# Kernel tuning notes

Measured on AMD Instinct MI355X. Metric: run time of the kernel, lower is better.

The kernel has to match this reference:

```python
import jax, jax.numpy as jnp
import numpy as np
import math

INC, OUTC, N, STRIDE = 128, 256, 9, 1
B, H, W = 8, 64, 64
EPS = 1e-5


def setup_inputs() -> dict:
    key = jax.random.key(0)
    k0, k1, k2, k3 = jax.random.split(key, 4)
    x = jax.random.normal(k0, (B, INC, H, W), jnp.float32)
    # p_conv: 3x3 conv inc -> 2N (torch inits weight=0; use small random so offsets are nontrivial)
    pw = jax.random.normal(k1, (2 * N, INC, 3, 3), jnp.float32) * 0.01
    pb = jax.random.normal(k2, (2 * N,), jnp.float32) * 0.01
    # final 1x1 conv inc -> outc (bias=None in the module), BN affine params
    cw = jax.random.normal(k3, (OUTC, INC, 1, 1), jnp.float32) * (1.0 / math.sqrt(INC))
    gamma = jnp.ones((OUTC,), jnp.float32)
    beta = jnp.zeros((OUTC,), jnp.float32)
    return dict(x=x, pw=pw, pb=pb, cw=cw, gamma=gamma, beta=beta)


def _akconv(x, pw, pb, cw, gamma, beta):
    b, c, Hx, Wx = x.shape
    # offset = p_conv(x): 3x3 conv, padding 1, stride STRIDE -> (b, 2N, h, w)
    offset = jax.lax.conv_general_dilated(
        x, pw, window_strides=(STRIDE, STRIDE), padding=((1, 1), (1, 1)),
        dimension_numbers=("NCHW", "OIHW", "NCHW")) + pb[None, :, None, None]
    h, w = offset.shape[2], offset.shape[3]

    # p_n: N points on unit circle (x=cos, y=sin), concat -> (2N,)
    angles = jnp.linspace(0.0, 2.0 * math.pi, N + 1)[:-1]
    p_n = jnp.concatenate([jnp.cos(angles), jnp.sin(angles)])  # (2N,)

    # p_0: base grid positions, (2N, h, w)
    gx = jnp.broadcast_to((jnp.arange(h, dtype=jnp.float32) * STRIDE)[:, None], (h, w))
    gy = jnp.broadcast_to((jnp.arange(w, dtype=jnp.float32) * STRIDE)[None, :], (h, w))
    p0 = jnp.concatenate([jnp.broadcast_to(gx[None], (N, h, w)),
                          jnp.broadcast_to(gy[None], (N, h, w))], axis=0)

    p = (offset + p_n[None, :, None, None] + p0[None]).transpose(0, 2, 3, 1)  # (b,h,w,2N)
    px, py = p[..., :N], p[..., N:]

    fx = jnp.floor(jax.lax.stop_gradient(px))  # q is detached in the original
    fy = jnp.floor(jax.lax.stop_gradient(py))
    q_ltx = jnp.clip(fx, 0, Hx - 1)
    q_lty = jnp.clip(fy, 0, Wx - 1)
    q_rbx = jnp.clip(fx + 1.0, 0, Hx - 1)
    q_rby = jnp.clip(fy + 1.0, 0, Wx - 1)
    pxc = jnp.clip(px, 0, Hx - 1)
    pyc = jnp.clip(py, 0, Wx - 1)

    g_lt = (1.0 + (q_ltx - pxc)) * (1.0 + (q_lty - pyc))
    g_rb = (1.0 - (q_rbx - pxc)) * (1.0 - (q_rby - pyc))
    g_lb = (1.0 + (q_ltx - pxc)) * (1.0 - (q_rby - pyc))
    g_rt = (1.0 - (q_rbx - pxc)) * (1.0 + (q_lty - pyc))

    x_flat = x.reshape(b, c, Hx * Wx)

    def gather(qx, qy):
        idx = (qx * Wx + qy).astype(jnp.int32).reshape(b, -1)  # (b, h*w*N)
        xg = jax.vmap(lambda xf, ix: xf[:, ix])(x_flat, idx)    # (b, c, h*w*N)
        return xg.reshape(b, c, h, w, N)

    x_off = (g_lt[:, None] * gather(q_ltx, q_lty)
             + g_rb[:, None] * gather(q_rbx, q_rby)
             + g_lb[:, None] * gather(q_ltx, q_rby)
             + g_rt[:, None] * gather(q_rbx, q_lty))  # (b,c,h,w,N)

    x_off = x_off.reshape(b, c, h, w * N)  # 'b c h w n -> b c h (w n)'

    # 1x1 conv (no bias) + BatchNorm (training-mode batch stats) + SiLU
    y = jnp.einsum("bchw,oc->bohw", x_off, cw[:, :, 0, 0])
    mean = jnp.mean(y, axis=(0, 2, 3), keepdims=True)
    var = jnp.var(y, axis=(0, 2, 3), keepdims=True)
    yn = (y - mean) * jax.lax.rsqrt(var + EPS)
    yn = yn * gamma[None, :, None, None] + beta[None, :, None, None]
    return yn * jax.nn.sigmoid(yn)


def reference(x, pw, pb, cw, gamma, beta):
    return _akconv(x, pw, pb, cw, gamma, beta)
```

## Files before the change

### kernel.cpp

```cpp
#include <hip/hip_runtime.h>
#include <math.h>

#define INC   128
#define OUTC  256
#define NPTS  9
#define BATCH 8
#define HDIM  64
#define WDIM  64
#define HW    4096
#define JLB   36864
#define JTOT  294912
#define NTOTF 294912.0f

typedef __bf16 bf16x8 __attribute__((ext_vector_type(8)));
typedef float  f32x4  __attribute__((ext_vector_type(4)));

__global__ void k_cvt_cw(const float* __restrict__ cw, __bf16* __restrict__ cwb) {
    int i = blockIdx.x * 256 + threadIdx.x;
    if (i < OUTC * INC) cwb[i] = (__bf16)cw[i];
}

__global__ __launch_bounds__(256) void k_transpose(
        const float* __restrict__ x, __bf16* __restrict__ xTb) {
    __shared__ __bf16 t[64 * 128];
    char* tb = (char*)t;
    int b   = blockIdx.x >> 6;
    int hw0 = (blockIdx.x & 63) << 6;
    int tid = threadIdx.x;
    int lane = tid & 63;
    int cq  = tid >> 6;
    const float* xb = x + b * (INC * HW);
    #pragma unroll
    for (int cc = 0; cc < INC; cc += 4) {
        int c = cc + cq;
        float v = xb[c * HW + hw0 + lane];
        *(__bf16*)(tb + lane * 256 + ((2 * c) ^ ((lane & 15) << 4))) = (__bf16)v;
    }
    __syncthreads();
    __bf16* ob = xTb + ((size_t)b * HW + hw0) * INC;
    #pragma unroll
    for (int i = 0; i < 4; ++i) {
        int chunk = i * 256 + tid;
        int hw  = chunk >> 4;
        int c16 = chunk & 15;
        bf16x8 vv = *(bf16x8*)(tb + hw * 256 + ((c16 * 16) ^ ((hw & 15) << 4)));
        *(bf16x8*)(ob + hw * INC + c16 * 8) = vv;
    }
}

__global__ __launch_bounds__(256) void k_prep(
        const float* __restrict__ x, const float* __restrict__ pw,
        const float* __restrict__ pb, int4* __restrict__ sidx,
        float4* __restrict__ sw) {
    int n  = blockIdx.x >> 7;
    int sp = ((blockIdx.x & 127) << 8) + threadIdx.x;
    int b  = sp >> 12;
    int hh = (sp >> 6) & 63;
    int ww = sp & 63;

    __shared__ float pwl[INC * 9 * 2];
    for (int i = threadIdx.x; i < INC * 9; i += 256) {
        pwl[i * 2 + 0] = pw[n * (INC * 9) + i];
        pwl[i * 2 + 1] = pw[(n + 9) * (INC * 9) + i];
    }
    __syncthreads();

    const float* xb = x + b * (INC * HW);
    float ax = 0.f, ay = 0.f;
    for (int c = 0; c < INC; ++c) {
        const float* xc = xb + c * HW;
        const float* pc = pwl + c * 18;
        #pragma unroll
        for (int ky = 0; ky < 3; ++ky) {
            int yy = hh - 1 + ky;
            #pragma unroll
            for (int kx = 0; kx < 3; ++kx) {
                int xx = ww - 1 + kx;
                float v = ((unsigned)yy < 64u && (unsigned)xx < 64u)
                            ? xc[yy * 64 + xx] : 0.f;
                int k = ky * 3 + kx;
                ax = fmaf(v, pc[k * 2 + 0], ax);
                ay = fmaf(v, pc[k * 2 + 1], ay);
            }
        }
    }
    ax += pb[n];
    ay += pb[n + 9];

    const float TWO_PI = 6.28318530717958647692f;
    float ang = (float)n * (TWO_PI / 9.0f);
    float px = ax + cosf(ang) + (float)hh;
    float py = ay + sinf(ang) + (float)ww;
    float fx = floorf(px), fy = floorf(py);
    float ltx = fminf(fmaxf(fx,        0.f), 63.f);
    float lty = fminf(fmaxf(fy,        0.f), 63.f);
    float rbx = fminf(fmaxf(fx + 1.f,  0.f), 63.f);
    float rby = fminf(fmaxf(fy + 1.f,  0.f), 63.f);
    float pxc = fminf(fmaxf(px,        0.f), 63.f);
    float pyc = fminf(fmaxf(py,        0.f), 63.f);
    float glt = (1.f + ltx - pxc) * (1.f + lty - pyc);
    float grb = (1.f - rbx + pxc) * (1.f - rby + pyc);
    float glb = (1.f + ltx - pxc) * (1.f - rby + pyc);
    float grt = (1.f - rbx + pxc) * (1.f + lty - pyc);

    int j = b * JLB + (hh * 64 + ww) * 9 + n;
    sidx[j] = make_int4((int)ltx * 64 + (int)lty,
                        (int)rbx * 64 + (int)rby,
                        (int)ltx * 64 + (int)rby,
                        (int)rbx * 64 + (int)lty);
    sw[j] = make_float4(glt, grb, glb, grt);
}

template <bool WRITE>
__global__ __launch_bounds__(256, 2) void k_gemm(
        const __bf16* __restrict__ xTb, const __bf16* __restrict__ cwb,
        const int4* __restrict__ sidx, const float4* __restrict__ sw,
        const float* __restrict__ scaleb, const float* __restrict__ shiftb,
        float* __restrict__ gstat, float* __restrict__ out) {
    __shared__ uint4 xoffT4[64 * 256 / 16];
    __shared__ float saux[512];
    char* xoffT = (char*)xoffT4;

    int bidx = blockIdx.x;
    int b    = bidx / 576;
    int jl0  = (bidx % 576) * 64;
    int tid  = threadIdx.x;
    int w    = tid >> 6;
    int l    = tid & 63;

    int col = tid >> 2;
    int q   = tid & 3;
    int j   = b * JLB + jl0 + col;
    int4   qi = sidx[j];
    float4 qw = sw[j];
    const __bf16* xtb = xTb + (size_t)b * (HW * INC) + q * 32;

    float accc[32];
    #pragma unroll
    for (int i = 0; i < 32; ++i) accc[i] = 0.f;

    const int   idx4[4] = { qi.x, qi.y, qi.z, qi.w };
    const float wt4[4]  = { qw.x, qw.y, qw.z, qw.w };
    #pragma unroll
    for (int p = 0; p < 4; ++p) {
        const __bf16* rp = xtb + idx4[p] * INC;
        float wp = wt4[p];
        #pragma unroll
        for (int v = 0; v < 4; ++v) {
            bf16x8 vv = *(const bf16x8*)(rp + v * 8);
            #pragma unroll
            for (int i = 0; i < 8; ++i)
                accc[v * 8 + i] = fmaf(wp, (float)vv[i], accc[v * 8 + i]);
        }
    }
    #pragma unroll
    for (int i8 = 0; i8 < 4; ++i8) {
        bf16x8 pk;
        #pragma unroll
        for (int i = 0; i < 8; ++i) pk[i] = (__bf16)accc[i8 * 8 + i];
        int colbyte = (q * 64 + i8 * 16) ^ ((col & 7) << 4);
        *(bf16x8*)(xoffT + col * 256 + colbyte) = pk;
    }

    if (WRITE) {
        saux[tid]       = scaleb[tid];
        saux[256 + tid] = shiftb[tid];
    }

    bf16x8 afrag[4][4];
    #pragma unroll
    for (int mt = 0; mt < 4; ++mt) {
        int m = w * 64 + mt * 16 + (l & 15);
        #pragma unroll
        for (int ks = 0; ks < 4; ++ks) {
            int k = ks * 32 + (l >> 4) * 8;
            afrag[mt][ks] = *(const bf16x8*)(cwb + m * 128 + k);
        }
    }

    __syncthreads();

    f32x4 acc[4][4] = {};
    #pragma unroll
    for (int ks = 0; ks < 4; ++ks) {
        bf16x8 bfrag[4];
        #pragma unroll
        for (int nt = 0; nt < 4; ++nt) {
            int row = nt * 16 + (l & 15);
            int colbyte = (ks * 64 + (l >> 4) * 16) ^ ((row & 7) << 4);
            bfrag[nt] = *(const bf16x8*)(xoffT + row * 256 + colbyte);
        }
        #pragma unroll
        for (int mt = 0; mt < 4; ++mt)
            #pragma unroll
            for (int nt = 0; nt < 4; ++nt)
                acc[mt][nt] = __builtin_amdgcn_mfma_f32_16x16x32_bf16(
                    afrag[mt][ks], bfrag[nt], acc[mt][nt], 0, 0, 0);
    }

    if (WRITE) {
        float* outb = out + (size_t)b * (OUTC * JLB);
        #pragma unroll
        for (int mt = 0; mt < 4; ++mt) {
            #pragma unroll
            for (int r = 0; r < 4; ++r) {
                int o = w * 64 + mt * 16 + (l >> 4) * 4 + r;
                float sc = saux[o];
                float sh = saux[256 + o];
                float* orow = outb + (size_t)o * JLB + jl0 + (l & 15);
                #pragma unroll
                for (int nt = 0; nt < 4; ++nt) {
                    float yn = fmaf(acc[mt][nt][r], sc, sh);
                    float so = yn / (1.f + __expf(-yn));
                    orow[nt * 16] = so;
                }
            }
        }
    } else {
        float* ssum = saux;
        float* ssq  = saux + 256;
        #pragma unroll
        for (int mt = 0; mt < 4; ++mt) {
            #pragma unroll
            for (int r = 0; r < 4; ++r) {
                float s = 0.f, qq = 0.f;
                #pragma unroll
                for (int nt = 0; nt < 4; ++nt) {
                    float v = acc[mt][nt][r];
                    s += v;
                    qq += v * v;
                }
                #pragma unroll
                for (int d = 1; d < 16; d <<= 1) {
                    s  += __shfl_xor(s, d, 64);
                    qq += __shfl_xor(qq, d, 64);
                }
                if ((l & 15) == 0) {
                    int row = w * 64 + mt * 16 + (l >> 4) * 4 + r;
                    ssum[row] = s;
                    ssq[row]  = qq;
                }
            }
        }
        __syncthreads();
        float* gs = gstat + (bidx & 63) * 512;
        atomicAdd(gs + tid,       ssum[tid]);
        atomicAdd(gs + 256 + tid, ssq[tid]);
    }
}

__global__ void k_stats(const float* __restrict__ gstat,
                        const float* __restrict__ gamma,
                        const float* __restrict__ beta,
                        float* __restrict__ scaleb, float* __restrict__ shiftb) {
    int t = threadIdx.x;
    float s = 0.f, q = 0.f;
    for (int r = 0; r < 64; ++r) {
        s += gstat[r * 512 + t];
        q += gstat[r * 512 + 256 + t];
    }
    float mean = s / NTOTF;
    float var  = q / NTOTF - mean * mean;
    float rstd = rsqrtf(var + 1e-5f);
    float sc = rstd * gamma[t];
    scaleb[t] = sc;
    shiftb[t] = beta[t] - mean * sc;
}

extern "C" void kernel_launch(void* const* d_in, const int* in_sizes, int n_in,
                              void* d_out, int out_size, void* d_ws, size_t ws_size,
                              hipStream_t stream) {
    (void)in_sizes; (void)n_in; (void)out_size; (void)ws_size;
    const float* x     = (const float*)d_in[0];
    const float* pw    = (const float*)d_in[1];
    const float* pb    = (const float*)d_in[2];
    const float* cw    = (const float*)d_in[3];
    const float* gamma = (const float*)d_in[4];
    const float* beta  = (const float*)d_in[5];
    float* out = (float*)d_out;

    char* ws = (char*)d_ws;
    __bf16* xTb   = (__bf16*)(ws);
    int4*   sidx  = (int4*)(ws + 8388608);
    float4* swt   = (float4*)(ws + 13107200);
    __bf16* cwb   = (__bf16*)(ws + 17825792);
    float*  gstat = (float*)(ws + 17891328);
    float*  scaleb= (float*)(ws + 18022400);
    float*  shiftb= (float*)(ws + 18023424);

    hipMemsetAsync(gstat, 0, 64 * 512 * 4, stream);
    k_cvt_cw<<<128, 256, 0, stream>>>(cw, cwb);
    k_transpose<<<512, 256, 0, stream>>>(x, xTb);
    k_prep<<<9 * 128, 256, 0, stream>>>(x, pw, pb, sidx, swt);
    k_gemm<false><<<4608, 256, 0, stream>>>(xTb, cwb, sidx, swt,
                                            nullptr, nullptr, gstat, nullptr);
    k_stats<<<1, 256, 0, stream>>>(gstat, gamma, beta, scaleb, shiftb);
    k_gemm<true><<<4608, 256, 0, stream>>>(xTb, cwb, sidx, swt,
                                           scaleb, shiftb, gstat, out);
}
```

Before: 223.6 us.

## Materialize gathered offset tile in workspace to skip regather in output pass

The first GEMM pass now also writes its bilinearly gathered bf16 x_off tile to a global workspace buffer (about 75 MB). A new output kernel loads that tile straight into LDS with global_load_lds and runs the MFMA GEMM plus BN/SiLU epilogue, so the second pass no longer redoes the four-way gather and interpolation. This trades the scattered gather reads for an extra sequential write and read of the x_off buffer. The path is used only when the workspace is large enough; otherwise the old two-pass recompute is kept.

```diff
diff --git a/kernel.cpp b/kernel.cpp
--- a/kernel.cpp
+++ b/kernel.cpp
@@ -14,6 +14,12 @@
 
 typedef __bf16 bf16x8 __attribute__((ext_vector_type(8)));
 typedef float  f32x4  __attribute__((ext_vector_type(4)));
+
+__device__ __forceinline__ void load_lds16(const void* g, void* lds) {
+    __builtin_amdgcn_global_load_lds(
+        (const __attribute__((address_space(1))) unsigned int*)g,
+        (__attribute__((address_space(3))) unsigned int*)lds, 16, 0, 0);
+}
 
 __global__ void k_cvt_cw(const float* __restrict__ cw, __bf16* __restrict__ cwb) {
     int i = blockIdx.x * 256 + threadIdx.x;
@@ -111,12 +117,13 @@
     sw[j] = make_float4(glt, grb, glb, grt);
 }
 
-template <bool WRITE>
+template <bool WRITE, bool XOFF>
 __global__ __launch_bounds__(256, 2) void k_gemm(
         const __bf16* __restrict__ xTb, const __bf16* __restrict__ cwb,
         const int4* __restrict__ sidx, const float4* __restrict__ sw,
         const float* __restrict__ scaleb, const float* __restrict__ shiftb,
-        float* __restrict__ gstat, float* __restrict__ out) {
+        float* __restrict__ gstat, float* __restrict__ out,
+        __bf16* __restrict__ xoffG) {
     __shared__ uint4 xoffT4[64 * 256 / 16];
     __shared__ float saux[512];
     char* xoffT = (char*)xoffT4;
@@ -153,6 +160,7 @@
                 accc[v * 8 + i] = fmaf(wp, (float)vv[i], accc[v * 8 + i]);
         }
     }
+    char* xg = XOFF ? ((char*)xoffG + (size_t)bidx * 16384) : nullptr;
     #pragma unroll
     for (int i8 = 0; i8 < 4; ++i8) {
         bf16x8 pk;
@@ -160,6 +168,8 @@
         for (int i = 0; i < 8; ++i) pk[i] = (__bf16)accc[i8 * 8 + i];
         int colbyte = (q * 64 + i8 * 16) ^ ((col & 7) << 4);
         *(bf16x8*)(xoffT + col * 256 + colbyte) = pk;
+        if (XOFF)
+            *(bf16x8*)(xg + col * 256 + colbyte) = pk;
     }
 
     if (WRITE) {
@@ -227,7 +237,7 @@
                 #pragma unroll
                 for (int nt = 0; nt < 4; ++nt) {
                     float v = acc[mt][nt][r];
-                    s += v;
+                    s  += v;
                     qq += v * v;
                 }
                 #pragma unroll
@@ -249,6 +259,80 @@
     }
 }
 
+__global__ __launch_bounds__(256, 2) void k_out(
+        const __bf16* __restrict__ xoffG, const __bf16* __restrict__ cwb,
+        const float* __restrict__ scaleb, const float* __restrict__ shiftb,
+        float* __restrict__ out) {
+    __shared__ uint4 xoffT4[64 * 256 / 16];
+    __shared__ float saux[512];
+    char* xoffT = (char*)xoffT4;
+
+    int bidx = blockIdx.x;
+    int b    = bidx / 576;
+    int jl0  = (bidx % 576) * 64;
+    int tid  = threadIdx.x;
+    int w    = tid >> 6;
+    int l    = tid & 63;
+
+    const char* gsrc = (const char*)xoffG + (size_t)bidx * 16384 + w * 4096;
+    char*       ldst = xoffT + w * 4096;
+    #pragma unroll
+    for (int it = 0; it < 4; ++it)
+        load_lds16(gsrc + it * 1024 + l * 16, ldst + it * 1024);
+
+    saux[tid]       = scaleb[tid];
+    saux[256 + tid] = shiftb[tid];
+
+    bf16x8 afrag[4][4];
+    #pragma unroll
+    for (int mt = 0; mt < 4; ++mt) {
+        int m = w * 64 + mt * 16 + (l & 15);
+        #pragma unroll
+        for (int ks = 0; ks < 4; ++ks) {
+            int k = ks * 32 + (l >> 4) * 8;
+            afrag[mt][ks] = *(const bf16x8*)(cwb + m * 128 + k);
+        }
+    }
+
+    __syncthreads();
+
+    f32x4 acc[4][4] = {};
+    #pragma unroll
+    for (int ks = 0; ks < 4; ++ks) {
+        bf16x8 bfrag[4];
+        #pragma unroll
+        for (int nt = 0; nt < 4; ++nt) {
+            int row = nt * 16 + (l & 15);
+            int colbyte = (ks * 64 + (l >> 4) * 16) ^ ((row & 7) << 4);
+            bfrag[nt] = *(const bf16x8*)(xoffT + row * 256 + colbyte);
+        }
+        #pragma unroll
+        for (int mt = 0; mt < 4; ++mt)
+            #pragma unroll
+            for (int nt = 0; nt < 4; ++nt)
+                acc[mt][nt] = __builtin_amdgcn_mfma_f32_16x16x32_bf16(
+                    afrag[mt][ks], bfrag[nt], acc[mt][nt], 0, 0, 0);
+    }
+
+    float* outb = out + (size_t)b * (OUTC * JLB);
+    #pragma unroll
+    for (int mt = 0; mt < 4; ++mt) {
+        #pragma unroll
+        for (int r = 0; r < 4; ++r) {
+            int o = w * 64 + mt * 16 + (l >> 4) * 4 + r;
+            float sc = saux[o];
+            float sh = saux[256 + o];
+            float* orow = outb + (size_t)o * JLB + jl0 + (l & 15);
+            #pragma unroll
+            for (int nt = 0; nt < 4; ++nt) {
+                float yn = fmaf(acc[mt][nt][r], sc, sh);
+                float so = yn / (1.f + __expf(-yn));
+                orow[nt * 16] = so;
+            }
+        }
+    }
+}
+
 __global__ void k_stats(const float* __restrict__ gstat,
                         const float* __restrict__ gamma,
                         const float* __restrict__ beta,
@@ -270,7 +354,7 @@
 extern "C" void kernel_launch(void* const* d_in, const int* in_sizes, int n_in,
                               void* d_out, int out_size, void* d_ws, size_t ws_size,
                               hipStream_t stream) {
-    (void)in_sizes; (void)n_in; (void)out_size; (void)ws_size;
+    (void)in_sizes; (void)n_in; (void)out_size;
     const float* x     = (const float*)d_in[0];
     const float* pw    = (const float*)d_in[1];
     const float* pb    = (const float*)d_in[2];
@@ -280,21 +364,33 @@
     float* out = (float*)d_out;
 
     char* ws = (char*)d_ws;
-    __bf16* xTb   = (__bf16*)(ws);
-    int4*   sidx  = (int4*)(ws + 8388608);
-    float4* swt   = (float4*)(ws + 13107200);
-    __bf16* cwb   = (__bf16*)(ws + 17825792);
-    float*  gstat = (float*)(ws + 17891328);
-    float*  scaleb= (float*)(ws + 18022400);
-    float*  shiftb= (float*)(ws + 18023424);
+    const size_t XOFF_BYTES = (size_t)4608 * 16384;
+    bool big = ws_size >= (XOFF_BYTES + 18087936ull);
+
+    size_t off = big ? XOFF_BYTES : 0;
+    __bf16* xoffG = (__bf16*)ws;
+    __bf16* xTb   = (__bf16*)(ws + off);
+    int4*   sidx  = (int4*)(ws + off + 8388608);
+    float4* swt   = (float4*)(ws + off + 13107200);
+    __bf16* cwb   = (__bf16*)(ws + off + 17825792);
+    float*  gstat = (float*)(ws + off + 17891328);
+    float*  scaleb= (float*)(ws + off + 18022400);
+    float*  shiftb= (float*)(ws + off + 18023424);
 
     hipMemsetAsync(gstat, 0, 64 * 512 * 4, stream);
     k_cvt_cw<<<128, 256, 0, stream>>>(cw, cwb);
     k_transpose<<<512, 256, 0, stream>>>(x, xTb);
     k_prep<<<9 * 128, 256, 0, stream>>>(x, pw, pb, sidx, swt);
-    k_gemm<false><<<4608, 256, 0, stream>>>(xTb, cwb, sidx, swt,
-                                            nullptr, nullptr, gstat, nullptr);
-    k_stats<<<1, 256, 0, stream>>>(gstat, gamma, beta, scaleb, shiftb);
-    k_gemm<true><<<4608, 256, 0, stream>>>(xTb, cwb, sidx, swt,
-                                           scaleb, shiftb, gstat, out);
-}
+    if (big) {
+        k_gemm<false, true><<<4608, 256, 0, stream>>>(
+            xTb, cwb, sidx, swt, nullptr, nullptr, gstat, nullptr, xoffG);
+        k_stats<<<1, 256, 0, stream>>>(gstat, gamma, beta, scaleb, shiftb);
+        k_out<<<4608, 256, 0, stream>>>(xoffG, cwb, scaleb, shiftb, out);
+    } else {
+        k_gemm<false, false><<<4608, 256, 0, stream>>>(
+            xTb, cwb, sidx, swt, nullptr, nullptr, gstat, nullptr, nullptr);
+        k_stats<<<1, 256, 0, stream>>>(gstat, gamma, beta, scaleb, shiftb);
+        k_gemm<true, false><<<4608, 256, 0, stream>>>(
+            xTb, cwb, sidx, swt, scaleb, shiftb, gstat, out, nullptr);
+    }
+}
```

Result: slower. 244.8 us (+9.5%).
